# Optimization experiments

Measured on AMD Instinct MI355X. Metric: run time of the kernel, lower is better.

Reference implementation:

```python
import jax, jax.numpy as jnp
import numpy as np
from jax import lax

BN_EPS = 1e-5

def conv1d(x, w, b):
    # x: [B,C,L], w: [O,I,K], padding 'same' for k=3
    y = lax.conv_general_dilated(x, w, window_strides=(1,), padding=[(1, 1)],
                                 dimension_numbers=("NCH", "OIH", "NCH"))
    return y + b[None, :, None]

def bn_eval(x, g, b, m, v):
    return (x - m[None, :, None]) / jnp.sqrt(v[None, :, None] + BN_EPS) * g[None, :, None] + b[None, :, None]

def maxpool2(x):
    B, C, L = x.shape
    return x.reshape(B, C, L // 2, 2).max(axis=-1)

def expert_block(x, w, b, g, be, m, v):
    return maxpool2(jax.nn.relu(bn_eval(conv1d(x, w, b), g, be, m, v)))

def setup_inputs() -> dict:
    key = jax.random.key(0)
    ks = jax.random.split(key, 40)
    B, L, E, C = 1024, 2048, 4, 5
    d = {"x": jax.random.normal(ks[0], (B, 1, L), jnp.float32)}
    d["conv1_w"] = jax.random.normal(ks[1], (8, 1, 3), jnp.float32) * 0.2
    d["conv1_b"] = jax.random.normal(ks[2], (8,), jnp.float32) * 0.02
    # stacked expert params, leading dim = num_experts
    chans = [(16, 8), (32, 16), (64, 32)]
    i = 3
    for blk, (co, ci) in enumerate(chans, start=1):
        d[f"ew{blk}"] = jax.random.normal(ks[i], (E, co, ci, 3), jnp.float32) * (1.0 / np.sqrt(ci * 3)); i += 1
        d[f"eb{blk}"] = jax.random.normal(ks[i], (E, co), jnp.float32) * 0.02; i += 1
        d[f"ebn{blk}_g"] = 0.5 + jax.random.uniform(ks[i], (E, co), jnp.float32); i += 1
        d[f"ebn{blk}_b"] = jax.random.normal(ks[i], (E, co), jnp.float32) * 0.02; i += 1
        d[f"ebn{blk}_m"] = jax.random.normal(ks[i], (E, co), jnp.float32) * 0.1; i += 1
        d[f"ebn{blk}_v"] = 0.5 + jax.random.uniform(ks[i], (E, co), jnp.float32); i += 1
    d["router_w"] = jax.random.normal(ks[i], (E, 8), jnp.float32) * 0.3; i += 1
    d["router_b"] = jnp.zeros((E,), jnp.float32)
    final_length = L // 8 * 64
    d["fc1_w"] = jax.random.normal(ks[i], (64, final_length), jnp.float32) * 0.01; i += 1
    d["fc1_b"] = jnp.zeros((64,), jnp.float32)
    d["fc2_w"] = jax.random.normal(ks[i], (C, 64), jnp.float32) * 0.1; i += 1
    d["fc2_b"] = jnp.zeros((C,), jnp.float32)
    return d

TOP_K = 2

def reference(x, conv1_w, conv1_b,
              ew1, eb1, ebn1_g, ebn1_b, ebn1_m, ebn1_v,
              ew2, eb2, ebn2_g, ebn2_b, ebn2_m, ebn2_v,
              ew3, eb3, ebn3_g, ebn3_b, ebn3_m, ebn3_v,
              router_w, router_b, fc1_w, fc1_b, fc2_w, fc2_b):
    B = x.shape[0]
    E = router_w.shape[0]
    h = jax.nn.relu(conv1d(x, conv1_w, conv1_b))           # [B,8,L]
    pooled = h.mean(axis=-1)                               # [B,8] (AdaptiveAvgPool1d(1))
    logits = pooled @ router_w.T + router_b                # [B,E]
    probs = jax.nn.softmax(logits, axis=-1)
    topk_gates, topk_idx = lax.top_k(probs, TOP_K)         # [B,K]
    topk_gates = topk_gates / topk_gates.sum(axis=-1, keepdims=True)
    # dense gate matrix [B,E]: zero where expert not in top-k
    onehot = jax.nn.one_hot(topk_idx, E, dtype=h.dtype)    # [B,K,E]
    gate = (topk_gates[..., None] * onehot).sum(axis=1)    # [B,E]
    # run every expert on the full batch (mathematically identical combine)
    def run_expert(p):
        w1, b1, g1, be1, m1, v1, w2, b2, g2, be2, m2, v2, w3, b3, g3, be3, m3, v3 = p
        o = expert_block(h, w1, b1, g1, be1, m1, v1)
        o = expert_block(o, w2, b2, g2, be2, m2, v2)
        o = expert_block(o, w3, b3, g3, be3, m3, v3)
        return o                                           # [B,64,L//8]
    eparams = (ew1, eb1, ebn1_g, ebn1_b, ebn1_m, ebn1_v,
               ew2, eb2, ebn2_g, ebn2_b, ebn2_m, ebn2_v,
               ew3, eb3, ebn3_g, ebn3_b, ebn3_m, ebn3_v)
    expert_outs = jax.vmap(run_expert)(eparams)            # [E,B,64,L//8]
    combined = jnp.einsum("ebcl,be->bcl", expert_outs, gate)
    flat = combined.reshape(B, -1)
    z = jax.nn.relu(flat @ fc1_w.T + fc1_b)                # dropout inactive in eval
    out = z @ fc2_w.T + fc2_b
    mean_probs = probs.mean(axis=0)
    cv = jnp.std(mean_probs, ddof=1) / (mean_probs.mean() + 1e-10)
    aux_loss = cv ** 2
    return out, aux_loss
```

## Files before the change

kernel.cpp:

```cpp
#include <hip/hip_runtime.h>

constexpr int L0 = 2048;
constexpr size_t OFF_POOLED = 0;
constexpr size_t OFF_TOPKI  = 8192;
constexpr size_t OFF_TOPKG  = 10240;
constexpr size_t OFF_B1     = 12288;
constexpr size_t OFF_B2     = 12352;
constexpr size_t OFF_B3     = 12480;
constexpr size_t OFF_W1P    = 12800;
constexpr size_t OFF_W2P    = 14848;
constexpr size_t OFF_W3P    = 23040;
constexpr size_t OFF_COMB   = 57344;
constexpr size_t OFF_P      = 57344 + 16777216;

__global__ __launch_bounds__(256) void pool_kernel(const float* __restrict__ x,
    const float* __restrict__ c1w, const float* __restrict__ c1b, float* __restrict__ pooled)
{
    __shared__ float xbuf[2050];
    __shared__ float red[8 * 256];
    int b = blockIdx.x, tid = threadIdx.x;
    const float* xr = x + (size_t)b * L0;
    for (int i = tid; i < 2050; i += 256) xbuf[i] = (i >= 1 && i <= L0) ? xr[i - 1] : 0.f;
    __syncthreads();
    float w[24], bb[8];
#pragma unroll
    for (int i = 0; i < 24; i++) w[i] = c1w[i];
#pragma unroll
    for (int c = 0; c < 8; c++) bb[c] = c1b[c];
    float acc[8];
#pragma unroll
    for (int c = 0; c < 8; c++) acc[c] = 0.f;
    for (int l = tid; l < L0; l += 256) {
        float xm = xbuf[l], x0 = xbuf[l + 1], xp = xbuf[l + 2];
#pragma unroll
        for (int c = 0; c < 8; c++)
            acc[c] += fmaxf(fmaf(w[3 * c], xm, fmaf(w[3 * c + 1], x0, fmaf(w[3 * c + 2], xp, bb[c]))), 0.f);
    }
#pragma unroll
    for (int c = 0; c < 8; c++) red[c * 256 + tid] = acc[c];
    __syncthreads();
    for (int off = 128; off > 0; off >>= 1) {
        if (tid < off) {
#pragma unroll
            for (int c = 0; c < 8; c++) red[c * 256 + tid] += red[c * 256 + tid + off];
        }
        __syncthreads();
    }
    if (tid < 8) pooled[b * 8 + tid] = red[tid * 256] * (1.f / L0);
}

__global__ __launch_bounds__(256) void repack_kernel(
    const float* __restrict__ ew1, const float* __restrict__ eb1, const float* __restrict__ g1,
    const float* __restrict__ bb1, const float* __restrict__ m1, const float* __restrict__ v1,
    const float* __restrict__ ew2, const float* __restrict__ eb2, const float* __restrict__ g2,
    const float* __restrict__ bb2, const float* __restrict__ m2, const float* __restrict__ v2,
    const float* __restrict__ ew3, const float* __restrict__ eb3, const float* __restrict__ g3,
    const float* __restrict__ bb3, const float* __restrict__ m3, const float* __restrict__ v3,
    float* __restrict__ w1p, float* __restrict__ w2p, float* __restrict__ w3p,
    float* __restrict__ b1p, float* __restrict__ b2p, float* __restrict__ b3p)
{
    int i = blockIdx.x * 256 + threadIdx.x;
    if (i < 2048) {
        int k = i & 3, r = i >> 2;
        int co = r & 15, r2 = r >> 4;
        int ci = r2 & 7, e = r2 >> 3;
        int ec = e * 16 + co;
        float A = g1[ec] * rsqrtf(v1[ec] + 1e-5f);
        w1p[i] = (k < 3) ? ew1[(ec * 8 + ci) * 3 + k] * A : 0.f;
    } else if (i < 10240) {
        int ii = i - 2048;
        int k = ii & 3, r = ii >> 2;
        int co = r & 31, r2 = r >> 5;
        int ci = r2 & 15, e = r2 >> 4;
        int ec = e * 32 + co;
        float A = g2[ec] * rsqrtf(v2[ec] + 1e-5f);
        w2p[ii] = (k < 3) ? ew2[(ec * 16 + ci) * 3 + k] * A : 0.f;
    } else if (i < 43008) {
        int ii = i - 10240;
        int k = ii & 3, r = ii >> 2;
        int co = r & 63, r2 = r >> 6;
        int ci = r2 & 31, e = r2 >> 5;
        int ec = e * 64 + co;
        float A = g3[ec] * rsqrtf(v3[ec] + 1e-5f);
        w3p[ii] = (k < 3) ? ew3[(ec * 32 + ci) * 3 + k] * A : 0.f;
    } else if (i < 43456) {
        int j = i - 43008;
        if (j < 64)       { float A = g1[j] * rsqrtf(v1[j] + 1e-5f); b1p[j] = fmaf(eb1[j] - m1[j], A, bb1[j]); }
        else if (j < 192) { int q = j - 64;  float A = g2[q] * rsqrtf(v2[q] + 1e-5f); b2p[q] = fmaf(eb2[q] - m2[q], A, bb2[q]); }
        else              { int q = j - 192; float A = g3[q] * rsqrtf(v3[q] + 1e-5f); b3p[q] = fmaf(eb3[q] - m3[q], A, bb3[q]); }
    }
}

__global__ __launch_bounds__(1024) void router_kernel(const float* __restrict__ pooled,
    const float* __restrict__ rw, const float* __restrict__ rb,
    int* __restrict__ tidx, float* __restrict__ tg, float* __restrict__ aux)
{
    __shared__ float pr[4][1024];
    int b = threadIdx.x;
    float p[8];
#pragma unroll
    for (int c = 0; c < 8; c++) p[c] = pooled[b * 8 + c];
    float lg[4];
#pragma unroll
    for (int e = 0; e < 4; e++) {
        float a = rb[e];
#pragma unroll
        for (int c = 0; c < 8; c++) a = fmaf(p[c], rw[e * 8 + c], a);
        lg[e] = a;
    }
    float m = fmaxf(fmaxf(lg[0], lg[1]), fmaxf(lg[2], lg[3]));
    float pe[4]; float s = 0.f;
#pragma unroll
    for (int e = 0; e < 4; e++) { pe[e] = expf(lg[e] - m); s += pe[e]; }
    float inv = 1.f / s;
#pragma unroll
    for (int e = 0; e < 4; e++) pe[e] *= inv;
    int e0 = 0;
#pragma unroll
    for (int e = 1; e < 4; e++) if (pe[e] > pe[e0]) e0 = e;
    int e1 = -1;
#pragma unroll
    for (int e = 0; e < 4; e++) if (e != e0 && (e1 < 0 || pe[e] > pe[e1])) e1 = e;
    float s2 = pe[e0] + pe[e1];
    tidx[b * 2] = e0; tidx[b * 2 + 1] = e1;
    tg[b * 2] = pe[e0] / s2; tg[b * 2 + 1] = pe[e1] / s2;
#pragma unroll
    for (int e = 0; e < 4; e++) pr[e][b] = pe[e];
    __syncthreads();
    for (int off = 512; off > 0; off >>= 1) {
        if (b < off) {
#pragma unroll
            for (int e = 0; e < 4; e++) pr[e][b] += pr[e][b + off];
        }
        __syncthreads();
    }
    if (b == 0) {
        float mp[4]; float mm = 0.f;
#pragma unroll
        for (int e = 0; e < 4; e++) { mp[e] = pr[e][0] * (1.f / 1024.f); mm += mp[e]; }
        mm *= 0.25f;
        float var = 0.f;
#pragma unroll
        for (int e = 0; e < 4; e++) { float d = mp[e] - mm; var += d * d; }
        var *= (1.f / 3.f);
        float cv = sqrtf(var) / (mm + 1e-10f);
        aux[0] = cv * cv;
    }
}

constexpr int XB_OFF = 0;
constexpr int E0_OFF = 288;
constexpr int O0_OFF = 1472;
constexpr int E1_OFF = 2656;
constexpr int O1_OFF = 3872;
constexpr int E2_OFF = 5088;
constexpr int O2_OFF = 6240;
constexpr int LDS_FLOATS = 7392;

#define DO_C(c, W) \
    aE[c][0] = fmaf(W.x, ev.x, fmaf(W.y, ov.x, fmaf(W.z, ev.y, aE[c][0]))); \
    aO[c][0] = fmaf(W.x, ov.x, fmaf(W.y, ev.y, fmaf(W.z, ov.y, aO[c][0]))); \
    aE[c][1] = fmaf(W.x, ev.y, fmaf(W.y, ov.y, fmaf(W.z, ev.z, aE[c][1]))); \
    aO[c][1] = fmaf(W.x, ov.y, fmaf(W.y, ev.z, fmaf(W.z, ov.z, aO[c][1]))); \
    aE[c][2] = fmaf(W.x, ev.z, fmaf(W.y, ov.z, fmaf(W.z, ev.w, aE[c][2]))); \
    aO[c][2] = fmaf(W.x, ov.z, fmaf(W.y, ev.w, fmaf(W.z, ov.w, aO[c][2]))); \
    aE[c][3] = fmaf(W.x, ev.w, fmaf(W.y, ov.w, fmaf(W.z, e4, aE[c][3]))); \
    aO[c][3] = fmaf(W.x, ov.w, fmaf(W.y, e4, fmaf(W.z, o4, aO[c][3])));

template<int CI, int CO, int SIN, int SOUT, int LOUT, int JOUT, bool GUARD>
__device__ __forceinline__ void stage2ch(
    const float* __restrict__ wp, const float b0, const float b1,
    const float* __restrict__ Ein, const float* __restrict__ Oin,
    float* __restrict__ Eout, float* __restrict__ Oout,
    const int a_out, const int co0, const int j0)
{
    float aE[2][4], aO[2][4];
#pragma unroll
    for (int p = 0; p < 4; ++p) { aE[0][p] = b0; aO[0][p] = b0; aE[1][p] = b1; aO[1][p] = b1; }
#pragma unroll 4
    for (int ci = 0; ci < CI; ++ci) {
        const float* wb = wp + (ci * CO + co0) * 4;
        float4 w0 = *reinterpret_cast<const float4*>(wb);
        float4 w1 = *reinterpret_cast<const float4*>(wb + 4);
        const float* ep = Ein + ci * SIN + j0;
        float4 ev = *reinterpret_cast<const float4*>(ep);
        float e4 = ep[4];
        const float* op = Oin + ci * SIN + j0;
        float4 ov = *reinterpret_cast<const float4*>(op);
        float o4 = op[4];
        DO_C(0, w0) DO_C(1, w1)
    }
#pragma unroll
    for (int c = 0; c < 2; ++c) {
        float v[4];
#pragma unroll
        for (int p = 0; p < 4; ++p) {
            int l = a_out + j0 + p;
            bool ok = (l >= 0) && (l < LOUT);
            if (GUARD) ok = ok && (j0 + p < JOUT);
            v[p] = ok ? fmaxf(fmaxf(aE[c][p], aO[c][p]), 0.f) : 0.f;
        }
        *reinterpret_cast<float2*>(Eout + (co0 + c) * SOUT + (j0 >> 1)) = make_float2(v[0], v[2]);
        *reinterpret_cast<float2*>(Oout + (co0 + c) * SOUT + (j0 >> 1)) = make_float2(v[1], v[3]);
    }
}

__device__ __forceinline__ void stage3_2ch(
    const float* __restrict__ wp, const float b0, const float b1,
    const float* __restrict__ Ein, const float* __restrict__ Oin,
    const float g, float oa[2][4], const int co0, const int j0)
{
    float aE[2][4], aO[2][4];
#pragma unroll
    for (int p = 0; p < 4; ++p) { aE[0][p] = b0; aO[0][p] = b0; aE[1][p] = b1; aO[1][p] = b1; }
#pragma unroll 4
    for (int ci = 0; ci < 32; ++ci) {
        const float* wb = wp + (ci * 64 + co0) * 4;
        float4 w0 = *reinterpret_cast<const float4*>(wb);
        float4 w1 = *reinterpret_cast<const float4*>(wb + 4);
        const float* ep = Ein + ci * 36 + j0;
        float4 ev = *reinterpret_cast<const float4*>(ep);
        float e4 = ep[4];
        const float* op = Oin + ci * 36 + j0;
        float4 ov = *reinterpret_cast<const float4*>(op);
        float o4 = op[4];
        DO_C(0, w0) DO_C(1, w1)
    }
#pragma unroll
    for (int c = 0; c < 2; ++c)
#pragma unroll
        for (int p = 0; p < 4; ++p)
            oa[c][p] = fmaf(g, fmaxf(fmaxf(aE[c][p], aO[c][p]), 0.f), oa[c][p]);
}

__global__ __launch_bounds__(256, 5) void expert_kernel(
    const float* __restrict__ x, const float* __restrict__ c1w, const float* __restrict__ c1b,
    const float* __restrict__ w1p, const float* __restrict__ w2p, const float* __restrict__ w3p,
    const float* __restrict__ b1p, const float* __restrict__ b2p, const float* __restrict__ b3p,
    const int* __restrict__ tidx, const float* __restrict__ tg,
    float* __restrict__ comb)
{
    __shared__ __align__(16) float lds[LDS_FLOATS];
    const int tid = threadIdx.x;
    const int bt = blockIdx.x;
    const int b = bt >> 3, t = bt & 7;
    const int a3 = t * 32, a2 = 2 * a3 - 1, a1 = 4 * a3 - 3, a0 = 8 * a3 - 7;
    const float* xr = x + (size_t)b * L0;
    float* xb = lds + XB_OFF;
    for (int m = tid; m < 284; m += 256) {
        int gpos = a0 - 1 + m;
        xb[m] = (gpos >= 0 && gpos < L0) ? xr[gpos] : 0.f;
    }
    __syncthreads();
    {
        const int ch = tid & 7;
        const int pj = tid >> 3;
        float wa = c1w[ch * 3], wb = c1w[ch * 3 + 1], wc = c1w[ch * 3 + 2], bc = c1b[ch];
        float* tgt = lds + ((pj & 1) ? O0_OFF : E0_OFF) + ch * 148;
        const int kb = pj >> 1;
        for (int k = 0; k < 9; ++k) {
            int j = pj + 32 * k;
            if (j >= 282) break;
            int l = a0 + j;
            float v = 0.f;
            if (l >= 0 && l < L0)
                v = fmaxf(fmaf(wa, xb[j], fmaf(wb, xb[j + 1], fmaf(wc, xb[j + 2], bc))), 0.f);
            tgt[kb + 16 * k] = v;
        }
    }
    const int ea = tidx[b * 2], eb2i = tidx[b * 2 + 1];
    const float ga = tg[b * 2], gb2 = tg[b * 2 + 1];
    const int cg1 = tid & 7,  pg1 = tid >> 3;
    const int cg2 = tid & 15, pg2 = tid >> 4;
    const int cg3 = tid >> 3, pg3 = tid & 7;
    const int co1 = 2 * cg1, co2 = 2 * cg2, co3 = 2 * cg3;
    const int j3 = 4 * pg3;
    float oa[2][4];
#pragma unroll
    for (int c = 0; c < 2; c++)
#pragma unroll
        for (int p = 0; p < 4; p++) oa[c][p] = 0.f;
#pragma unroll 1
    for (int slot = 0; slot < 2; ++slot) {
        const int e = slot ? eb2i : ea;
        const float g = slot ? gb2 : ga;
        __syncthreads();
        {
            const float* wp = w1p + e * 512;
            float2 bb = *reinterpret_cast<const float2*>(b1p + e * 16 + co1);
            stage2ch<8, 16, 148, 76, 1024, 138, false>(wp, bb.x, bb.y,
                lds + E0_OFF, lds + O0_OFF, lds + E1_OFF, lds + O1_OFF, a1, co1, 4 * pg1);
            if (pg1 < 3)
                stage2ch<8, 16, 148, 76, 1024, 138, true>(wp, bb.x, bb.y,
                    lds + E0_OFF, lds + O0_OFF, lds + E1_OFF, lds + O1_OFF, a1, co1, 128 + 4 * pg1);
        }
        __syncthreads();
        {
            const float* wp = w2p + e * 2048;
            float2 bb = *reinterpret_cast<const float2*>(b2p + e * 32 + co2);
            stage2ch<16, 32, 76, 36, 512, 66, false>(wp, bb.x, bb.y,
                lds + E1_OFF, lds + O1_OFF, lds + E2_OFF, lds + O2_OFF, a2, co2, 4 * pg2);
            if (pg2 == 0)
                stage2ch<16, 32, 76, 36, 512, 66, true>(wp, bb.x, bb.y,
                    lds + E1_OFF, lds + O1_OFF, lds + E2_OFF, lds + O2_OFF, a2, co2, 64);
        }
        __syncthreads();
        {
            const float* wp = w3p + e * 8192;
            float2 bb = *reinterpret_cast<const float2*>(b3p + e * 64 + co3);
            stage3_2ch(wp, bb.x, bb.y, lds + E2_OFF, lds + O2_OFF, g, oa, co3, j3);
        }
    }
    float* cb = comb + (size_t)b * 16384 + (size_t)co3 * 256 + a3 + j3;
    *reinterpret_cast<float4*>(cb)       = make_float4(oa[0][0], oa[0][1], oa[0][2], oa[0][3]);
    *reinterpret_cast<float4*>(cb + 256) = make_float4(oa[1][0], oa[1][1], oa[1][2], oa[1][3]);
}

__global__ __launch_bounds__(256) void fc1_kernel(const float* __restrict__ comb,
    const float* __restrict__ w, float* __restrict__ P)
{
    __shared__ __align__(16) float at[64 * 65];
    __shared__ __align__(16) float wt[64 * 65];
    int bc = blockIdx.x;
    int kc = blockIdx.y;
    int tid = threadIdx.x;
    int tx = tid & 15, ty = tid >> 4;
    float acc[4][4];
#pragma unroll
    for (int i = 0; i < 4; i++)
#pragma unroll
        for (int j = 0; j < 4; j++) acc[i][j] = 0.f;
    int b0 = bc * 64;
    for (int kt = 0; kt < 32; ++kt) {
        int k0 = kc * 2048 + kt * 64;
        __syncthreads();
        for (int i = tid; i < 4096; i += 256) {
            int r = i >> 6, kk = i & 63;
            at[r * 65 + kk] = comb[(size_t)(b0 + r) * 16384 + k0 + kk];
            wt[r * 65 + kk] = w[(size_t)r * 16384 + k0 + kk];
        }
        __syncthreads();
#pragma unroll 8
        for (int kk = 0; kk < 64; kk++) {
            float av[4], wv[4];
#pragma unroll
            for (int i = 0; i < 4; i++) av[i] = at[(ty * 4 + i) * 65 + kk];
#pragma unroll
            for (int j = 0; j < 4; j++) wv[j] = wt[(tx * 4 + j) * 65 + kk];
#pragma unroll
            for (int i = 0; i < 4; i++)
#pragma unroll
                for (int j = 0; j < 4; j++) acc[i][j] = fmaf(av[i], wv[j], acc[i][j]);
        }
    }
    float* Pp = P + (size_t)kc * 65536;
#pragma unroll
    for (int i = 0; i < 4; i++)
#pragma unroll
        for (int j = 0; j < 4; j++)
            Pp[(size_t)(b0 + ty * 4 + i) * 64 + tx * 4 + j] = acc[i][j];
}

__global__ __launch_bounds__(256) void fc2_kernel(const float* __restrict__ P,
    const float* __restrict__ f1b, const float* __restrict__ w2, const float* __restrict__ b2,
    float* __restrict__ out)
{
    int b = blockIdx.x * 256 + threadIdx.x;
    float z[64];
#pragma unroll
    for (int n = 0; n < 64; n++) z[n] = 0.f;
    for (int kc = 0; kc < 8; kc++) {
        const float* Pp = P + (size_t)kc * 65536 + (size_t)b * 64;
#pragma unroll
        for (int n = 0; n < 64; n++) z[n] += Pp[n];
    }
    float o[5] = {0.f, 0.f, 0.f, 0.f, 0.f};
#pragma unroll
    for (int n = 0; n < 64; n++) {
        float zz = fmaxf(z[n] + f1b[n], 0.f);
#pragma unroll
        for (int c = 0; c < 5; c++) o[c] = fmaf(zz, w2[c * 64 + n], o[c]);
    }
#pragma unroll
    for (int c = 0; c < 5; c++) out[b * 5 + c] = o[c] + b2[c];
}

extern "C" void kernel_launch(void* const* d_in, const int* in_sizes, int n_in,
                              void* d_out, int out_size, void* d_ws, size_t ws_size,
                              hipStream_t stream)
{
    const float* x   = (const float*)d_in[0];
    const float* c1w = (const float*)d_in[1];
    const float* c1b = (const float*)d_in[2];
    const float* ew1 = (const float*)d_in[3];
    const float* eb1 = (const float*)d_in[4];
    const float* g1  = (const float*)d_in[5];
    const float* bb1 = (const float*)d_in[6];
    const float* m1  = (const float*)d_in[7];
    const float* v1  = (const float*)d_in[8];
    const float* ew2 = (const float*)d_in[9];
    const float* eb2 = (const float*)d_in[10];
    const float* g2  = (const float*)d_in[11];
    const float* bb2 = (const float*)d_in[12];
    const float* m2  = (const float*)d_in[13];
    const float* v2  = (const float*)d_in[14];
    const float* ew3 = (const float*)d_in[15];
    const float* eb3 = (const float*)d_in[16];
    const float* g3  = (const float*)d_in[17];
    const float* bb3 = (const float*)d_in[18];
    const float* m3  = (const float*)d_in[19];
    const float* v3  = (const float*)d_in[20];
    const float* rw  = (const float*)d_in[21];
    const float* rb  = (const float*)d_in[22];
    const float* f1w = (const float*)d_in[23];
    const float* f1b = (const float*)d_in[24];
    const float* f2w = (const float*)d_in[25];
    const float* f2b = (const float*)d_in[26];

    float* ws     = (float*)d_ws;
    float* pooled = ws + OFF_POOLED;
    int*   tidx   = (int*)(ws + OFF_TOPKI);
    float* tg     = ws + OFF_TOPKG;
    float* b1p    = ws + OFF_B1;
    float* b2p    = ws + OFF_B2;
    float* b3p    = ws + OFF_B3;
    float* w1p    = ws + OFF_W1P;
    float* w2p    = ws + OFF_W2P;
    float* w3p    = ws + OFF_W3P;
    float* comb   = ws + OFF_COMB;
    float* P      = ws + OFF_P;
    float* out    = (float*)d_out;

    hipLaunchKernelGGL(pool_kernel, dim3(1024), dim3(256), 0, stream, x, c1w, c1b, pooled);
    hipLaunchKernelGGL(repack_kernel, dim3(170), dim3(256), 0, stream,
                       ew1, eb1, g1, bb1, m1, v1, ew2, eb2, g2, bb2, m2, v2,
                       ew3, eb3, g3, bb3, m3, v3, w1p, w2p, w3p, b1p, b2p, b3p);
    hipLaunchKernelGGL(router_kernel, dim3(1), dim3(1024), 0, stream, pooled, rw, rb, tidx, tg, out + 5120);
    hipLaunchKernelGGL(expert_kernel, dim3(8192), dim3(256), 0, stream,
                       x, c1w, c1b, w1p, w2p, w3p, b1p, b2p, b3p, tidx, tg, comb);
    hipLaunchKernelGGL(fc1_kernel, dim3(16, 8), dim3(256), 0, stream, comb, f1w, P);
    hipLaunchKernelGGL(fc2_kernel, dim3(4), dim3(256), 0, stream, P, f1b, f2w, f2b, out);
}
```

Baseline: 501.1 us.

## Remap expert conv to one channel by eight positions, split fc1 K further

```diff
diff --git a/kernel.cpp b/kernel.cpp
--- a/kernel.cpp
+++ b/kernel.cpp
@@ -7,9 +7,9 @@
 constexpr size_t OFF_B1     = 12288;
 constexpr size_t OFF_B2     = 12352;
 constexpr size_t OFF_B3     = 12480;
-constexpr size_t OFF_W1P    = 12800;
-constexpr size_t OFF_W2P    = 14848;
-constexpr size_t OFF_W3P    = 23040;
+constexpr size_t OFF_W1Q    = 12800;
+constexpr size_t OFF_W2Q    = 14848;
+constexpr size_t OFF_W3Q    = 23040;
 constexpr size_t OFF_COMB   = 57344;
 constexpr size_t OFF_P      = 57344 + 16777216;
 
@@ -17,7 +17,7 @@
     const float* __restrict__ c1w, const float* __restrict__ c1b, float* __restrict__ pooled)
 {
     __shared__ float xbuf[2050];
-    __shared__ float red[8 * 256];
+    __shared__ float part[4][8];
     int b = blockIdx.x, tid = threadIdx.x;
     const float* xr = x + (size_t)b * L0;
     for (int i = tid; i < 2050; i += 256) xbuf[i] = (i >= 1 && i <= L0) ? xr[i - 1] : 0.f;
@@ -37,16 +37,21 @@
             acc[c] += fmaxf(fmaf(w[3 * c], xm, fmaf(w[3 * c + 1], x0, fmaf(w[3 * c + 2], xp, bb[c]))), 0.f);
     }
 #pragma unroll
-    for (int c = 0; c < 8; c++) red[c * 256 + tid] = acc[c];
+    for (int c = 0; c < 8; c++) {
+#pragma unroll
+        for (int off = 32; off > 0; off >>= 1)
+            acc[c] += __shfl_down(acc[c], off, 64);
+    }
+    int wv = tid >> 6, ln = tid & 63;
+    if (ln == 0) {
+#pragma unroll
+        for (int c = 0; c < 8; c++) part[wv][c] = acc[c];
+    }
     __syncthreads();
-    for (int off = 128; off > 0; off >>= 1) {
-        if (tid < off) {
-#pragma unroll
-            for (int c = 0; c < 8; c++) red[c * 256 + tid] += red[c * 256 + tid + off];
-        }
-        __syncthreads();
-    }
-    if (tid < 8) pooled[b * 8 + tid] = red[tid * 256] * (1.f / L0);
+    if (tid < 8) {
+        float s = part[0][tid] + part[1][tid] + part[2][tid] + part[3][tid];
+        pooled[b * 8 + tid] = s * (1.f / L0);
+    }
 }
 
 __global__ __launch_bounds__(256) void repack_kernel(
@@ -56,33 +61,27 @@
     const float* __restrict__ bb2, const float* __restrict__ m2, const float* __restrict__ v2,
     const float* __restrict__ ew3, const float* __restrict__ eb3, const float* __restrict__ g3,
     const float* __restrict__ bb3, const float* __restrict__ m3, const float* __restrict__ v3,
-    float* __restrict__ w1p, float* __restrict__ w2p, float* __restrict__ w3p,
+    float* __restrict__ w1q, float* __restrict__ w2q, float* __restrict__ w3q,
     float* __restrict__ b1p, float* __restrict__ b2p, float* __restrict__ b3p)
 {
     int i = blockIdx.x * 256 + threadIdx.x;
     if (i < 2048) {
-        int k = i & 3, r = i >> 2;
-        int co = r & 15, r2 = r >> 4;
-        int ci = r2 & 7, e = r2 >> 3;
+        int k = i & 3, ci = (i >> 2) & 7, co = (i >> 5) & 15, e = i >> 9;
         int ec = e * 16 + co;
         float A = g1[ec] * rsqrtf(v1[ec] + 1e-5f);
-        w1p[i] = (k < 3) ? ew1[(ec * 8 + ci) * 3 + k] * A : 0.f;
+        w1q[i] = (k < 3) ? ew1[(ec * 8 + ci) * 3 + k] * A : 0.f;
     } else if (i < 10240) {
         int ii = i - 2048;
-        int k = ii & 3, r = ii >> 2;
-        int co = r & 31, r2 = r >> 5;
-        int ci = r2 & 15, e = r2 >> 4;
+        int k = ii & 3, ci = (ii >> 2) & 15, co = (ii >> 6) & 31, e = ii >> 11;
         int ec = e * 32 + co;
         float A = g2[ec] * rsqrtf(v2[ec] + 1e-5f);
-        w2p[ii] = (k < 3) ? ew2[(ec * 16 + ci) * 3 + k] * A : 0.f;
+        w2q[ii] = (k < 3) ? ew2[(ec * 16 + ci) * 3 + k] * A : 0.f;
     } else if (i < 43008) {
         int ii = i - 10240;
-        int k = ii & 3, r = ii >> 2;
-        int co = r & 63, r2 = r >> 6;
-        int ci = r2 & 31, e = r2 >> 5;
+        int k = ii & 3, ci = (ii >> 2) & 31, co = (ii >> 7) & 63, e = ii >> 13;
         int ec = e * 64 + co;
         float A = g3[ec] * rsqrtf(v3[ec] + 1e-5f);
-        w3p[ii] = (k < 3) ? ew3[(ec * 32 + ci) * 3 + k] * A : 0.f;
+        w3q[ii] = (k < 3) ? ew3[(ec * 32 + ci) * 3 + k] * A : 0.f;
     } else if (i < 43456) {
         int j = i - 43008;
         if (j < 64)       { float A = g1[j] * rsqrtf(v1[j] + 1e-5f); b1p[j] = fmaf(eb1[j] - m1[j], A, bb1[j]); }
@@ -157,85 +156,57 @@
 constexpr int O2_OFF = 6240;
 constexpr int LDS_FLOATS = 7392;
 
-#define DO_C(c, W) \
-    aE[c][0] = fmaf(W.x, ev.x, fmaf(W.y, ov.x, fmaf(W.z, ev.y, aE[c][0]))); \
-    aO[c][0] = fmaf(W.x, ov.x, fmaf(W.y, ev.y, fmaf(W.z, ov.y, aO[c][0]))); \
-    aE[c][1] = fmaf(W.x, ev.y, fmaf(W.y, ov.y, fmaf(W.z, ev.z, aE[c][1]))); \
-    aO[c][1] = fmaf(W.x, ov.y, fmaf(W.y, ev.z, fmaf(W.z, ov.z, aO[c][1]))); \
-    aE[c][2] = fmaf(W.x, ev.z, fmaf(W.y, ov.z, fmaf(W.z, ev.w, aE[c][2]))); \
-    aO[c][2] = fmaf(W.x, ov.z, fmaf(W.y, ev.w, fmaf(W.z, ov.w, aO[c][2]))); \
-    aE[c][3] = fmaf(W.x, ev.w, fmaf(W.y, ov.w, fmaf(W.z, e4, aE[c][3]))); \
-    aO[c][3] = fmaf(W.x, ov.w, fmaf(W.y, e4, fmaf(W.z, o4, aO[c][3])));
-
-template<int CI, int CO, int SIN, int SOUT, int LOUT, int JOUT, bool GUARD>
-__device__ __forceinline__ void stage2ch(
-    const float* __restrict__ wp, const float b0, const float b1,
+template<int CI, int SIN>
+__device__ __forceinline__ void conv1ch8(
+    const float* __restrict__ wq,
+    const float bias,
     const float* __restrict__ Ein, const float* __restrict__ Oin,
+    const int j0, float vE[8], float vO[8])
+{
+#pragma unroll
+    for (int p = 0; p < 8; ++p) { vE[p] = bias; vO[p] = bias; }
+#pragma unroll
+    for (int ci = 0; ci < CI; ++ci) {
+        const float4 w = *reinterpret_cast<const float4*>(wq + ci * 4);
+        const float* ep = Ein + ci * SIN + j0;
+        const float4 ea = *reinterpret_cast<const float4*>(ep);
+        const float4 eb = *reinterpret_cast<const float4*>(ep + 4);
+        const float e8 = ep[8];
+        const float* op = Oin + ci * SIN + j0;
+        const float4 oa = *reinterpret_cast<const float4*>(op);
+        const float4 ob = *reinterpret_cast<const float4*>(op + 4);
+        const float o8 = op[8];
+        const float E[9] = {ea.x, ea.y, ea.z, ea.w, eb.x, eb.y, eb.z, eb.w, e8};
+        const float O[9] = {oa.x, oa.y, oa.z, oa.w, ob.x, ob.y, ob.z, ob.w, o8};
+#pragma unroll
+        for (int p = 0; p < 8; ++p) {
+            vE[p] = fmaf(w.x, E[p], fmaf(w.y, O[p], fmaf(w.z, E[p + 1], vE[p])));
+            vO[p] = fmaf(w.x, O[p], fmaf(w.y, E[p + 1], fmaf(w.z, O[p + 1], vO[p])));
+        }
+    }
+}
+
+template<int SOUT, int LOUT, bool GUARDJ>
+__device__ __forceinline__ void pool_store(
+    const float vE[8], const float vO[8],
     float* __restrict__ Eout, float* __restrict__ Oout,
-    const int a_out, const int co0, const int j0)
-{
-    float aE[2][4], aO[2][4];
-#pragma unroll
-    for (int p = 0; p < 4; ++p) { aE[0][p] = b0; aO[0][p] = b0; aE[1][p] = b1; aO[1][p] = b1; }
-#pragma unroll 4
-    for (int ci = 0; ci < CI; ++ci) {
-        const float* wb = wp + (ci * CO + co0) * 4;
-        float4 w0 = *reinterpret_cast<const float4*>(wb);
-        float4 w1 = *reinterpret_cast<const float4*>(wb + 4);
-        const float* ep = Ein + ci * SIN + j0;
-        float4 ev = *reinterpret_cast<const float4*>(ep);
-        float e4 = ep[4];
-        const float* op = Oin + ci * SIN + j0;
-        float4 ov = *reinterpret_cast<const float4*>(op);
-        float o4 = op[4];
-        DO_C(0, w0) DO_C(1, w1)
-    }
-#pragma unroll
-    for (int c = 0; c < 2; ++c) {
-        float v[4];
-#pragma unroll
-        for (int p = 0; p < 4; ++p) {
-            int l = a_out + j0 + p;
-            bool ok = (l >= 0) && (l < LOUT);
-            if (GUARD) ok = ok && (j0 + p < JOUT);
-            v[p] = ok ? fmaxf(fmaxf(aE[c][p], aO[c][p]), 0.f) : 0.f;
-        }
-        *reinterpret_cast<float2*>(Eout + (co0 + c) * SOUT + (j0 >> 1)) = make_float2(v[0], v[2]);
-        *reinterpret_cast<float2*>(Oout + (co0 + c) * SOUT + (j0 >> 1)) = make_float2(v[1], v[3]);
-    }
-}
-
-__device__ __forceinline__ void stage3_2ch(
-    const float* __restrict__ wp, const float b0, const float b1,
-    const float* __restrict__ Ein, const float* __restrict__ Oin,
-    const float g, float oa[2][4], const int co0, const int j0)
-{
-    float aE[2][4], aO[2][4];
-#pragma unroll
-    for (int p = 0; p < 4; ++p) { aE[0][p] = b0; aO[0][p] = b0; aE[1][p] = b1; aO[1][p] = b1; }
-#pragma unroll 4
-    for (int ci = 0; ci < 32; ++ci) {
-        const float* wb = wp + (ci * 64 + co0) * 4;
-        float4 w0 = *reinterpret_cast<const float4*>(wb);
-        float4 w1 = *reinterpret_cast<const float4*>(wb + 4);
-        const float* ep = Ein + ci * 36 + j0;
-        float4 ev = *reinterpret_cast<const float4*>(ep);
-        float e4 = ep[4];
-        const float* op = Oin + ci * 36 + j0;
-        float4 ov = *reinterpret_cast<const float4*>(op);
-        float o4 = op[4];
-        DO_C(0, w0) DO_C(1, w1)
-    }
-#pragma unroll
-    for (int c = 0; c < 2; ++c)
-#pragma unroll
-        for (int p = 0; p < 4; ++p)
-            oa[c][p] = fmaf(g, fmaxf(fmaxf(aE[c][p], aO[c][p]), 0.f), oa[c][p]);
+    const int co, const int j0, const int a_out, const int jmax)
+{
+    float v[8];
+#pragma unroll
+    for (int p = 0; p < 8; ++p) {
+        int l = a_out + j0 + p;
+        bool ok = (l >= 0) && (l < LOUT);
+        if (GUARDJ) ok = ok && (j0 + p < jmax);
+        v[p] = ok ? fmaxf(fmaxf(vE[p], vO[p]), 0.f) : 0.f;
+    }
+    *reinterpret_cast<float4*>(Eout + co * SOUT + (j0 >> 1)) = make_float4(v[0], v[2], v[4], v[6]);
+    *reinterpret_cast<float4*>(Oout + co * SOUT + (j0 >> 1)) = make_float4(v[1], v[3], v[5], v[7]);
 }
 
 __global__ __launch_bounds__(256, 5) void expert_kernel(
     const float* __restrict__ x, const float* __restrict__ c1w, const float* __restrict__ c1b,
-    const float* __restrict__ w1p, const float* __restrict__ w2p, const float* __restrict__ w3p,
+    const float* __restrict__ w1q, const float* __restrict__ w2q, const float* __restrict__ w3q,
     const float* __restrict__ b1p, const float* __restrict__ b2p, const float* __restrict__ b3p,
     const int* __restrict__ tidx, const float* __restrict__ tg,
     float* __restrict__ comb)
@@ -270,50 +241,54 @@
     }
     const int ea = tidx[b * 2], eb2i = tidx[b * 2 + 1];
     const float ga = tg[b * 2], gb2 = tg[b * 2 + 1];
-    const int cg1 = tid & 7,  pg1 = tid >> 3;
-    const int cg2 = tid & 15, pg2 = tid >> 4;
-    const int cg3 = tid >> 3, pg3 = tid & 7;
-    const int co1 = 2 * cg1, co2 = 2 * cg2, co3 = 2 * cg3;
-    const int j3 = 4 * pg3;
-    float oa[2][4];
-#pragma unroll
-    for (int c = 0; c < 2; c++)
-#pragma unroll
-        for (int p = 0; p < 4; p++) oa[c][p] = 0.f;
+    const int co1 = tid & 15, pg1 = tid >> 4;
+    const int co2 = tid & 31, pg2 = tid >> 5;
+    const int co3 = tid >> 2, pg3 = tid & 3;
+    const int j3 = 8 * pg3;
+    float oacc[8];
+#pragma unroll
+    for (int p = 0; p < 8; p++) oacc[p] = 0.f;
+    float vE[8], vO[8];
 #pragma unroll 1
     for (int slot = 0; slot < 2; ++slot) {
         const int e = slot ? eb2i : ea;
         const float g = slot ? gb2 : ga;
         __syncthreads();
         {
-            const float* wp = w1p + e * 512;
-            float2 bb = *reinterpret_cast<const float2*>(b1p + e * 16 + co1);
-            stage2ch<8, 16, 148, 76, 1024, 138, false>(wp, bb.x, bb.y,
-                lds + E0_OFF, lds + O0_OFF, lds + E1_OFF, lds + O1_OFF, a1, co1, 4 * pg1);
-            if (pg1 < 3)
-                stage2ch<8, 16, 148, 76, 1024, 138, true>(wp, bb.x, bb.y,
-                    lds + E0_OFF, lds + O0_OFF, lds + E1_OFF, lds + O1_OFF, a1, co1, 128 + 4 * pg1);
+            const float* wq = w1q + (size_t)(e * 16 + co1) * 32;
+            const float bias = b1p[e * 16 + co1];
+            conv1ch8<8, 148>(wq, bias, lds + E0_OFF, lds + O0_OFF, 8 * pg1, vE, vO);
+            pool_store<76, 1024, false>(vE, vO, lds + E1_OFF, lds + O1_OFF, co1, 8 * pg1, a1, 138);
+            if (pg1 < 2) {
+                int j0 = 128 + 8 * pg1;
+                conv1ch8<8, 148>(wq, bias, lds + E0_OFF, lds + O0_OFF, j0, vE, vO);
+                pool_store<76, 1024, true>(vE, vO, lds + E1_OFF, lds + O1_OFF, co1, j0, a1, 138);
+            }
         }
         __syncthreads();
         {
-            const float* wp = w2p + e * 2048;
-            float2 bb = *reinterpret_cast<const float2*>(b2p + e * 32 + co2);
-            stage2ch<16, 32, 76, 36, 512, 66, false>(wp, bb.x, bb.y,
-                lds + E1_OFF, lds + O1_OFF, lds + E2_OFF, lds + O2_OFF, a2, co2, 4 * pg2);
-            if (pg2 == 0)
-                stage2ch<16, 32, 76, 36, 512, 66, true>(wp, bb.x, bb.y,
-                    lds + E1_OFF, lds + O1_OFF, lds + E2_OFF, lds + O2_OFF, a2, co2, 64);
+            const float* wq = w2q + (size_t)(e * 32 + co2) * 64;
+            const float bias = b2p[e * 32 + co2];
+            conv1ch8<16, 76>(wq, bias, lds + E1_OFF, lds + O1_OFF, 8 * pg2, vE, vO);
+            pool_store<36, 512, false>(vE, vO, lds + E2_OFF, lds + O2_OFF, co2, 8 * pg2, a2, 66);
+            if (pg2 == 0) {
+                conv1ch8<16, 76>(wq, bias, lds + E1_OFF, lds + O1_OFF, 64, vE, vO);
+                pool_store<36, 512, true>(vE, vO, lds + E2_OFF, lds + O2_OFF, co2, 64, a2, 66);
+            }
         }
         __syncthreads();
         {
-            const float* wp = w3p + e * 8192;
-            float2 bb = *reinterpret_cast<const float2*>(b3p + e * 64 + co3);
-            stage3_2ch(wp, bb.x, bb.y, lds + E2_OFF, lds + O2_OFF, g, oa, co3, j3);
+            const float* wq = w3q + (size_t)(e * 64 + co3) * 128;
+            const float bias = b3p[e * 64 + co3];
+            conv1ch8<32, 36>(wq, bias, lds + E2_OFF, lds + O2_OFF, j3, vE, vO);
+#pragma unroll
+            for (int p = 0; p < 8; ++p)
+                oacc[p] = fmaf(g, fmaxf(fmaxf(vE[p], vO[p]), 0.f), oacc[p]);
         }
     }
     float* cb = comb + (size_t)b * 16384 + (size_t)co3 * 256 + a3 + j3;
-    *reinterpret_cast<float4*>(cb)       = make_float4(oa[0][0], oa[0][1], oa[0][2], oa[0][3]);
-    *reinterpret_cast<float4*>(cb + 256) = make_float4(oa[1][0], oa[1][1], oa[1][2], oa[1][3]);
+    *reinterpret_cast<float4*>(cb)     = make_float4(oacc[0], oacc[1], oacc[2], oacc[3]);
+    *reinterpret_cast<float4*>(cb + 4) = make_float4(oacc[4], oacc[5], oacc[6], oacc[7]);
 }
 
 __global__ __launch_bounds__(256) void fc1_kernel(const float* __restrict__ comb,
@@ -331,8 +306,8 @@
 #pragma unroll
         for (int j = 0; j < 4; j++) acc[i][j] = 0.f;
     int b0 = bc * 64;
-    for (int kt = 0; kt < 32; ++kt) {
-        int k0 = kc * 2048 + kt * 64;
+    for (int kt = 0; kt < 16; ++kt) {
+        int k0 = kc * 1024 + kt * 64;
         __syncthreads();
         for (int i = tid; i < 4096; i += 256) {
             int r = i >> 6, kk = i & 63;
@@ -361,15 +336,15 @@
             Pp[(size_t)(b0 + ty * 4 + i) * 64 + tx * 4 + j] = acc[i][j];
 }
 
-__global__ __launch_bounds__(256) void fc2_kernel(const float* __restrict__ P,
+__global__ __launch_bounds__(64) void fc2_kernel(const float* __restrict__ P,
     const float* __restrict__ f1b, const float* __restrict__ w2, const float* __restrict__ b2,
     float* __restrict__ out)
 {
-    int b = blockIdx.x * 256 + threadIdx.x;
+    int b = blockIdx.x * 64 + threadIdx.x;
     float z[64];
 #pragma unroll
     for (int n = 0; n < 64; n++) z[n] = 0.f;
-    for (int kc = 0; kc < 8; kc++) {
+    for (int kc = 0; kc < 16; kc++) {
         const float* Pp = P + (size_t)kc * 65536 + (size_t)b * 64;
 #pragma unroll
         for (int n = 0; n < 64; n++) z[n] += Pp[n];
@@ -424,9 +399,9 @@
     float* b1p    = ws + OFF_B1;
     float* b2p    = ws + OFF_B2;
     float* b3p    = ws + OFF_B3;
-    float* w1p    = ws + OFF_W1P;
-    float* w2p    = ws + OFF_W2P;
-    float* w3p    = ws + OFF_W3P;
+    float* w1q    = ws + OFF_W1Q;
+    float* w2q    = ws + OFF_W2Q;
+    float* w3q    = ws + OFF_W3Q;
     float* comb   = ws + OFF_COMB;
     float* P      = ws + OFF_P;
     float* out    = (float*)d_out;
@@ -434,10 +409,10 @@
     hipLaunchKernelGGL(pool_kernel, dim3(1024), dim3(256), 0, stream, x, c1w, c1b, pooled);
     hipLaunchKernelGGL(repack_kernel, dim3(170), dim3(256), 0, stream,
                        ew1, eb1, g1, bb1, m1, v1, ew2, eb2, g2, bb2, m2, v2,
-                       ew3, eb3, g3, bb3, m3, v3, w1p, w2p, w3p, b1p, b2p, b3p);
+                       ew3, eb3, g3, bb3, m3, v3, w1q, w2q, w3q, b1p, b2p, b3p);
     hipLaunchKernelGGL(router_kernel, dim3(1), dim3(1024), 0, stream, pooled, rw, rb, tidx, tg, out + 5120);
     hipLaunchKernelGGL(expert_kernel, dim3(8192), dim3(256), 0, stream,
-                       x, c1w, c1b, w1p, w2p, w3p, b1p, b2p, b3p, tidx, tg, comb);
-    hipLaunchKernelGGL(fc1_kernel, dim3(16, 8), dim3(256), 0, stream, comb, f1w, P);
-    hipLaunchKernelGGL(fc2_kernel, dim3(4), dim3(256), 0, stream, P, f1b, f2w, f2b, out);
-}
+                       x, c1w, c1b, w1q, w2q, w3q, b1p, b2p, b3p, tidx, tg, comb);
+    hipLaunchKernelGGL(fc1_kernel, dim3(16, 16), dim3(256), 0, stream, comb, f1w, P);
+    hipLaunchKernelGGL(fc2_kernel, dim3(16), dim3(64), 0, stream, P, f1b, f2w, f2b, out);
+}
```

New measurement: 409.8 us. -18.2%, faster.
